# Kernel tuning notes

Measured on AMD Instinct MI355X. Metric: run time of the kernel, lower is better.

## Reference

```python
import jax, jax.numpy as jnp
import numpy as np

B, S, P, H, W, TAG, M, K = 4, 2, 17, 128, 128, 1, 8, 10
PHW = P * H * W
SIGMA, SF = 0.2, 3.0
E_INV = float(np.e ** -1)
EPS = 1e-6


def setup_inputs() -> dict:
    key = jax.random.key(0)
    k1, k2, k3, k4, k5, k6, k7 = jax.random.split(key, 7)
    preds = jax.random.normal(k1, (B, S, (1 + TAG) * P, H, W), jnp.float32)
    gt_masks = jax.random.uniform(k2, (B, H, W), jnp.float32)
    gt_heatmaps = jax.random.uniform(k3, (B, P, H, W), jnp.float32)
    pos = jax.random.uniform(k4, (B, M, P, 2), jnp.float32) * H  # pixel coords
    vis = jax.random.randint(k5, (B, M, P, 1), 0, 2).astype(jnp.float32)
    gt_skeletons = jnp.concatenate([pos, vis], axis=-1)  # [B,M,P,3] = (x, y, vis)
    kp_idx = jax.random.randint(k6, (B, M, P, 1), 0, PHW)
    kp_vis = jax.random.randint(k7, (B, M, P, 1), 0, 2)
    gt_keypoints = jnp.concatenate([kp_idx, kp_vis], axis=-1).astype(jnp.int32)  # [B,M,J,2]
    return {"preds": preds, "gt_masks": gt_masks, "gt_heatmaps": gt_heatmaps,
            "gt_skeletons": gt_skeletons, "gt_keypoints": gt_keypoints}


def _clog(x):
    # torch BCE clamps log at -100
    return jnp.clip(jnp.log(x), -100.0, None)


def _tag_single(pt, kp):
    # pt: [TAG, PHW] tag map for one (image, stack); kp: [M, J, 2] int (flat_idx, vis)
    idx = kp[..., 0]
    vis = (kp[..., 1] > 0).astype(pt.dtype)  # [M, J]
    g = jnp.transpose(pt[:, idx], (1, 2, 0))  # [M, J, TAG]
    cnt = vis.sum(1)  # [M]
    valid = (cnt > 0).astype(pt.dtype)
    safe = jnp.maximum(cnt, 1.0)
    mean_tag = (g * vis[..., None]).sum(1) / safe[:, None]  # [M, TAG]
    # pull: per-person mean over (visible joints x tag dims) of squared deviation
    pull_pp = (((g - mean_tag[:, None]) ** 2) * vis[..., None]).sum((1, 2)) / (safe * TAG)
    num = valid.sum()
    pull = (pull_pp * valid).sum() / (num + EPS)
    d = ((mean_tag[:, None] - mean_tag[None]) ** 2).sum(-1)  # [M, M]
    pm = jnp.exp(-d) * valid[:, None] * valid[None]
    push = (pm.sum() - num) / ((num - 1.0) * num + EPS) * 0.5
    return push, pull


def _forward(preds, gt_masks, gt_heatmaps, gt_skeletons, gt_keypoints):
    hm = preds[:, :, :P]  # [B,S,P,H,W] raw heatmap logits
    prob = jax.nn.sigmoid(hm)
    # ---- detection loss (weighted BCE, per stack) ----
    t = (gt_heatmaps > E_INV).astype(jnp.float32)[:, None]  # [B,1,P,H,W]
    wgt = 10.0 * t + 0.5 * (gt_heatmaps < E_INV).astype(jnp.float32)[:, None]
    x = prob * gt_masks[:, None, None]
    bce = -(t * _clog(x) + (1.0 - t) * _clog(1.0 - x))
    det_loss = (wgt * bce).mean(axis=(0, 2, 3, 4))  # [S]
    # ---- associative embedding push/pull ----
    pred_tag_imgs = preds[:, :, P:(1 + TAG) * P].reshape(B, S, TAG, P, H, W)
    pred_tags = pred_tag_imgs.reshape(B, S, TAG, PHW)
    push, pull = jax.vmap(lambda ptb, kpb: jax.vmap(lambda pt: _tag_single(pt, kpb))(ptb))(
        pred_tags, gt_keypoints)  # each [B,S]
    # ---- keypoint sampling: top-K of flattened probability maps ----
    flat = prob.reshape(B, S, PHW)
    _, topi = jax.lax.top_k(flat, K)  # [B,S,K]
    part = topi // (H * W)
    rem = topi % (H * W)
    xi = rem // W
    yi = rem % W
    pos = jnp.stack([xi, yi], -1).astype(jnp.float32)  # [B,S,K,2]
    # ---- nearest-person matching (faithful to source, incl. vis==1 penalty) ----
    max_dist = float(H + W)
    sk_t = jnp.transpose(gt_skeletons, (0, 2, 1, 3))  # [B,P,M,3]
    pidx = jnp.broadcast_to(part.reshape(B, S * K)[:, :, None, None], (B, S * K, M, 3))
    sk_sel = jnp.take_along_axis(sk_t, pidx, axis=1).reshape(B, S, K, M, 3)
    vispen = max_dist * (sk_sel[..., 2] == 1).astype(jnp.float32)  # [B,S,K,M]
    dvec = vispen[..., None] + sk_sel[..., 1:] - pos[..., None, :]
    dist = jnp.sqrt((dvec ** 2).sum(-1) + 1e-12)
    person_ids = jnp.argmin(dist, axis=-1)  # [B,S,K]
    # ---- gather tag values at sampled locations ----
    pti = jnp.transpose(pred_tag_imgs, (0, 1, 3, 4, 5, 2))  # [B,S,P,H,W,TAG]
    bb = jnp.arange(B)[:, None, None]
    ss = jnp.arange(S)[None, :, None]
    tv = pti[bb, ss, part, xi, yi]  # [B,S,K,TAG]
    # ---- SkeletonGenerator: tag-conditioned soft-argmax ----
    aff = ((pti[:, :, None] - tv[:, :, :, None, None, None, :]) ** 2).sum(-1)  # [B,S,K,P,H,W]
    logits = SF * hm[:, :, None] - aff / (2.0 * SIGMA ** 2)
    wts = jax.nn.softmax(logits.reshape(B, S, K, P, H * W), -1).reshape(B, S, K, P, H, W)
    px = (wts * jnp.arange(H, dtype=jnp.float32)[:, None]).sum((-1, -2))  # [B,S,K,P]
    py = (wts * jnp.arange(W, dtype=jnp.float32)).sum((-1, -2))
    skel = jnp.stack([px, py], -1)  # [B,S,K,P,2]
    gts = gt_skeletons[bb, person_ids]  # [B,S,K,P,3]
    err = jnp.sqrt(((gts[..., :2] - skel) ** 2).sum(-1) + 1e-12) * (gts[..., 2] > 0)
    delta = 0.1
    a = jnp.abs(err)
    small = (a < delta).astype(jnp.float32)
    hub = small * err ** 2 + (1.0 - small) * delta * (a - delta / 2.0)
    skel_loss = hub.mean(-1).mean(-1)  # [B,S]
    # ---- weighted sum (loss_weights = (1,1,1,10)) ----
    return (1.0 * push.mean() + 1.0 * pull.mean() + 1.0 * det_loss.mean()
            + 10.0 * skel_loss.mean())


def reference(preds, gt_masks, gt_heatmaps, gt_skeletons, gt_keypoints):
    return _forward(preds, gt_masks, gt_heatmaps, gt_skeletons, gt_keypoints)
```

## Files before the change

### kernel.cpp

```cpp
#include <hip/hip_runtime.h>
#include <math.h>

#define B_ 4
#define S_ 2
#define P_ 17
#define H_ 128
#define W_ 128
#define M_ 8
#define K_ 10
#define HW_ (H_*W_)
#define PHW_ (P_*HW_)
#define CH_ 34
#define G_ 34
#define C_ (PHW_/G_)
#define E_INV_F 0.36787944117144233f
#define LOG2E 1.4426950408889634f
#define SF_ 3.0f
#define INV2SIG 12.5f
#define MAXDIST 256.0f

#define TOP1_BLOCKS (B_*S_*G_)
#define DET_BLOCKS  544
#define TAG_BLOCKS  (B_*S_)
#define MAIN_BLOCKS (TOP1_BLOCKS + DET_BLOCKS + TAG_BLOCKS)

#define SKEL_CHUNKS 4
#define NBSP (B_*S_*P_)
#define SKEL_BLOCKS (NBSP*SKEL_CHUNKS)

__device__ __forceinline__ unsigned int map32(float f) {
    unsigned int u = __float_as_uint(f);
    unsigned int flip = (unsigned int)((int)u >> 31) | 0x80000000u;
    return u ^ flip;
}

__device__ __forceinline__ void insert10(unsigned long long* a, unsigned long long key) {
    #pragma unroll
    for (int j = 9; j >= 1; --j) {
        unsigned long long am1 = a[j-1];
        a[j] = (key > am1) ? am1 : ((key > a[j]) ? key : a[j]);
    }
    a[0] = (key > a[0]) ? key : a[0];
}

__device__ __forceinline__ void merge10(unsigned long long* a, const unsigned long long* b) {
    #pragma unroll
    for (int t = 0; t < 10; ++t) {
        unsigned long long key = b[t];
        if (key > a[9]) insert10(a, key);
    }
}

__global__ __launch_bounds__(256, 4) void k_main(const float* __restrict__ preds,
                                                 const float* __restrict__ gmask,
                                                 const float* __restrict__ gh,
                                                 const int* __restrict__ kp,
                                                 unsigned long long* __restrict__ cand,
                                                 float* __restrict__ ws_det,
                                                 float* __restrict__ ws_tag) {
    int tid = threadIdx.x;
    if (blockIdx.x < TOP1_BLOCKS) {
        int bs = blockIdx.x / G_;
        int c  = blockIdx.x % G_;
        int wave = tid >> 6, lane = tid & 63;
        const float4* base = (const float4*)(preds + (size_t)bs*CH_*HW_ + (size_t)c*C_);
        unsigned long long a[10];
        #pragma unroll
        for (int j = 0; j < 10; ++j) a[j] = 0ull;
        for (int j = 0; j < 8; ++j) {
            int idx4 = wave*512 + j*64 + lane;
            float4 v = base[idx4];
            unsigned int i0 = (unsigned int)(c*C_ + idx4*4);
            const float* vv = &v.x;
            #pragma unroll
            for (int cc = 0; cc < 4; ++cc) {
                unsigned int key32 = map32(vv[cc]);
                unsigned int thr = (unsigned int)(a[9] >> 32);
                unsigned long long mask = __ballot(key32 >= thr);
                if (mask) {
                    unsigned long long kk =
                        ((unsigned long long)key32 << 32) | (unsigned int)(~(i0 + cc));
                    do {
                        int l = (int)__ffsll(mask) - 1;
                        unsigned long long cnd = __shfl(kk, l);
                        if (cnd > a[9]) insert10(a, cnd);
                        mask &= mask - 1;
                    } while (mask);
                }
            }
        }
        __shared__ unsigned long long smw[4][10];
        if (lane == 0) {
            #pragma unroll
            for (int j = 0; j < 10; ++j) smw[wave][j] = a[j];
        }
        __syncthreads();
        if (tid < 2) {
            unsigned long long x[10], y[10];
            #pragma unroll
            for (int j = 0; j < 10; ++j) { x[j] = smw[tid][j]; y[j] = smw[tid+2][j]; }
            merge10(x, y);
            #pragma unroll
            for (int j = 0; j < 10; ++j) smw[tid][j] = x[j];
        }
        __syncthreads();
        if (tid == 0) {
            unsigned long long x[10], y[10];
            #pragma unroll
            for (int j = 0; j < 10; ++j) { x[j] = smw[0][j]; y[j] = smw[1][j]; }
            merge10(x, y);
            #pragma unroll
            for (int j = 0; j < 10; ++j) cand[(size_t)blockIdx.x*10 + j] = x[j];
        }
    } else if (blockIdx.x < TOP1_BLOCKS + DET_BLOCKS) {
        int dblk = blockIdx.x - TOP1_BLOCKS;
        int t = dblk*256 + tid;
        float acc = 0.0f;
        #pragma unroll
        for (int j = 0; j < 4; ++j) {
            int q = t + j*(DET_BLOCKS*256);
            int hw4 = q & 4095;
            int t1  = q >> 12;
            int p   = t1 % P_;
            int t2  = t1 / P_;
            float4 hm4 = ((const float4*)preds)[(t2*CH_ + p)*4096 + hw4];
            float4 gm4 = ((const float4*)gmask)[(t2>>1)*4096 + hw4];
            float4 gh4 = ((const float4*)gh)[((t2>>1)*P_ + p)*4096 + hw4];
            const float* hmv = &hm4.x; const float* gmv = &gm4.x; const float* ghv4 = &gh4.x;
            #pragma unroll
            for (int cc = 0; cc < 4; ++cc) {
                float hm = hmv[cc];
                float e = exp2f(-fabsf(hm)*LOG2E);
                float r = __builtin_amdgcn_rcpf(1.0f + e);
                float prob = (hm >= 0.0f) ? r : e*r;
                float x = prob * gmv[cc];
                float ghv = ghv4[cc];
                float tt  = (ghv > E_INV_F) ? 1.0f : 0.0f;
                float wgt = 10.0f*tt + ((ghv < E_INV_F) ? 0.5f : 0.0f);
                float lx  = fmaxf(__logf(x),        -100.0f);
                float l1x = fmaxf(__logf(1.0f - x), -100.0f);
                acc += wgt * (-(tt*lx + (1.0f - tt)*l1x));
            }
        }
        #pragma unroll
        for (int off = 32; off > 0; off >>= 1) acc += __shfl_down(acc, off);
        __shared__ float sred[4];
        int wave = tid >> 6, lane = tid & 63;
        if (lane == 0) sred[wave] = acc;
        __syncthreads();
        if (tid == 0) ws_det[dblk] = sred[0] + sred[1] + sred[2] + sred[3];
    } else {
        int bs = blockIdx.x - (TOP1_BLOCKS + DET_BLOCKS);
        int b = bs / S_;
        __shared__ float g[M_*P_];
        __shared__ float vis[M_*P_];
        __shared__ float mean_tag[M_];
        __shared__ float validm[M_];
        __shared__ float pull_pp[M_];
        const float* tagbase = preds + ((size_t)bs*CH_ + P_)*HW_;
        if (tid < M_*P_) {
            int m = tid / P_; int p = tid % P_;
            int off = ((b*M_ + m)*P_ + p)*2;
            int idx = kp[off];
            int v   = kp[off+1];
            g[tid]   = tagbase[idx];
            vis[tid] = (v > 0) ? 1.0f : 0.0f;
        }
        __syncthreads();
        if (tid < M_) {
            float cnt = 0.0f, sum = 0.0f;
            for (int p = 0; p < P_; p++) { cnt += vis[tid*P_+p]; sum += g[tid*P_+p]*vis[tid*P_+p]; }
            float safe = fmaxf(cnt, 1.0f);
            float mt = sum / safe;
            mean_tag[tid] = mt;
            validm[tid] = (cnt > 0.0f) ? 1.0f : 0.0f;
            float pp = 0.0f;
            for (int p = 0; p < P_; p++) { float d = g[tid*P_+p] - mt; pp += d*d*vis[tid*P_+p]; }
            pull_pp[tid] = pp / safe;
        }
        __syncthreads();
        if (tid == 0) {
            float num = 0.0f;
            for (int m = 0; m < M_; m++) num += validm[m];
            float pull = 0.0f;
            for (int m = 0; m < M_; m++) pull += pull_pp[m]*validm[m];
            pull = pull / (num + 1e-6f);
            float pmsum = 0.0f;
            for (int i = 0; i < M_; i++)
                for (int j = 0; j < M_; j++) {
                    float d = mean_tag[i] - mean_tag[j]; d = d*d;
                    pmsum += expf(-d)*validm[i]*validm[j];
                }
            float push = (pmsum - num) / ((num - 1.0f)*num + 1e-6f) * 0.5f;
            ws_tag[bs] = push + pull;
        }
    }
}

__global__ __launch_bounds__(64) void k_top2(const float* __restrict__ preds,
                                             const float* __restrict__ gsk,
                                             const unsigned long long* __restrict__ cand,
                                             float* __restrict__ ws_tv,
                                             int* __restrict__ ws_pid) {
    int bs = blockIdx.x; int b = bs / S_;
    int tid = threadIdx.x;
    __shared__ unsigned long long sm[64*10];
    if (tid < G_) {
        #pragma unroll
        for (int j = 0; j < 10; ++j) sm[tid*10+j] = cand[((size_t)bs*G_ + tid)*10 + j];
    } else {
        #pragma unroll
        for (int j = 0; j < 10; ++j) sm[tid*10+j] = 0ull;
    }
    __syncthreads();
    for (int st = 32; st >= 1; st >>= 1) {
        if (tid < st) {
            unsigned long long x[10], y[10];
            #pragma unroll
            for (int j = 0; j < 10; ++j) { x[j] = sm[tid*10+j]; y[j] = sm[(tid+st)*10+j]; }
            merge10(x, y);
            #pragma unroll
            for (int j = 0; j < 10; ++j) sm[tid*10+j] = x[j];
        }
        __syncthreads();
    }
    if (tid < K_) {
        unsigned long long key = sm[tid];
        unsigned int topi = (unsigned int)(~key);
        int part = topi >> 14;
        int rem  = topi & (HW_-1);
        int xi   = rem >> 7;
        int yi   = rem & (W_-1);
        const float* tagbase = preds + ((size_t)bs*CH_ + P_)*HW_;
        float tv = tagbase[topi];
        float best = INFINITY; int pid = 0;
        for (int m = 0; m < M_; m++) {
            const float* sk = gsk + ((size_t)(b*M_ + m)*P_ + part)*3;
            float sk1 = sk[1], sk2 = sk[2];
            float vp = (sk2 == 1.0f) ? MAXDIST : 0.0f;
            float d0 = vp + sk1 - (float)xi;
            float d1 = vp + sk2 - (float)yi;
            float dist = sqrtf(d0*d0 + d1*d1 + 1e-12f);
            if (dist < best) { best = dist; pid = m; }
        }
        int o = bs*K_ + tid;
        ws_tv[o]  = tv;
        ws_pid[o] = pid;
    }
}

__global__ __launch_bounds__(256, 4) void k_skel(const float* __restrict__ preds,
                                                 const float* __restrict__ ws_tv,
                                                 float* __restrict__ ws_skl,
                                                 float* __restrict__ ws_ssx,
                                                 float* __restrict__ ws_ssy) {
    int bid   = blockIdx.x / SKEL_CHUNKS;
    int chunk = blockIdx.x % SKEL_CHUNKS;
    int p  = bid % P_;
    int bs = bid / P_;
    const float4* hm4 = (const float4*)(preds + ((size_t)bs*CH_ + p)*HW_);
    const float4* tg4 = (const float4*)(preds + ((size_t)bs*CH_ + P_ + p)*HW_);
    float tv[K_];
    #pragma unroll
    for (int k = 0; k < K_; k++) tv[k] = ws_tv[bs*K_ + k];
    float l[K_], sx[K_], sy[K_];
    #pragma unroll
    for (int k = 0; k < K_; k++) { l[k] = 0.0f; sx[k] = 0.0f; sy[k] = 0.0f; }
    int tid = threadIdx.x;
    const float C2 = INV2SIG * LOG2E;
    #pragma unroll
    for (int j = 0; j < 4; ++j) {
        int q = chunk*1024 + j*256 + tid;
        float4 hv = hm4[q];
        float4 tg = tg4[q];
        float h  = (float)(q >> 5);
        float w0 = (float)((q*4) & (W_-1));
        const float* hvv = &hv.x; const float* tgv = &tg.x;
        #pragma unroll
        for (int cc = 0; cc < 4; ++cc) {
            float a2 = (SF_*LOG2E) * hvv[cc];
            float tgc = tgv[cc];
            float w = w0 + (float)cc;
            #pragma unroll
            for (int k = 0; k < K_; k++) {
                float d = tgc - tv[k];
                float e = exp2f(fmaf(-C2, d*d, a2));
                l[k] += e;
                sx[k] = fmaf(e, h, sx[k]);
                sy[k] = fmaf(e, w, sy[k]);
            }
        }
    }
    #pragma unroll
    for (int k = 0; k < K_; k++) {
        for (int off = 32; off > 0; off >>= 1) {
            l[k]  += __shfl_down(l[k],  off);
            sx[k] += __shfl_down(sx[k], off);
            sy[k] += __shfl_down(sy[k], off);
        }
    }
    __shared__ float red[4][K_][3];
    int wave = tid >> 6, lane = tid & 63;
    if (lane == 0) {
        #pragma unroll
        for (int k = 0; k < K_; k++) {
            red[wave][k][0] = l[k]; red[wave][k][1] = sx[k]; red[wave][k][2] = sy[k];
        }
    }
    __syncthreads();
    if (tid < K_) {
        int k = tid;
        float L  = red[0][k][0] + red[1][k][0] + red[2][k][0] + red[3][k][0];
        float SX = red[0][k][1] + red[1][k][1] + red[2][k][1] + red[3][k][1];
        float SY = red[0][k][2] + red[1][k][2] + red[2][k][2] + red[3][k][2];
        int o = blockIdx.x*K_ + k;
        ws_skl[o] = L; ws_ssx[o] = SX; ws_ssy[o] = SY;
    }
}

__global__ __launch_bounds__(256) void k_fin(const float* __restrict__ gsk,
                                             const int* __restrict__ ws_pid,
                                             const float* __restrict__ ws_skl,
                                             const float* __restrict__ ws_ssx,
                                             const float* __restrict__ ws_ssy,
                                             const float* __restrict__ ws_det,
                                             const float* __restrict__ ws_tag,
                                             float* __restrict__ out) {
    int tid = threadIdx.x;
    float acc = 0.0f;
    for (int i = tid; i < DET_BLOCKS; i += 256) acc += ws_det[i];
    acc *= (1.0f/(float)(B_*S_*P_*HW_));
    if (tid < B_*S_) acc += ws_tag[tid] * (1.0f/(float)(B_*S_));
    for (int idx = tid; idx < NBSP*K_; idx += 256) {
        int bid = idx / K_;
        int k   = idx % K_;
        int p  = bid % P_;
        int bs = bid / P_;
        int b  = bs / S_;
        float L = 0.0f, SX = 0.0f, SY = 0.0f;
        #pragma unroll
        for (int c = 0; c < SKEL_CHUNKS; ++c) {
            int o = (bid*SKEL_CHUNKS + c)*K_ + k;
            L += ws_skl[o]; SX += ws_ssx[o]; SY += ws_ssy[o];
        }
        float px = SX / L, py = SY / L;
        int pid = ws_pid[bs*K_ + k];
        const float* g = gsk + ((size_t)(b*M_ + pid)*P_ + p)*3;
        float d0 = g[0] - px, d1 = g[1] - py;
        float gate = (g[2] > 0.0f) ? 1.0f : 0.0f;
        float err = sqrtf(d0*d0 + d1*d1 + 1e-12f) * gate;
        float hub = (err < 0.1f) ? err*err : 0.1f*(err - 0.05f);
        acc += hub * (10.0f/(float)(B_*S_*K_*P_));
    }
    #pragma unroll
    for (int off = 32; off > 0; off >>= 1) acc += __shfl_down(acc, off);
    __shared__ float sred[4];
    int wave = tid >> 6, lane = tid & 63;
    if (lane == 0) sred[wave] = acc;
    __syncthreads();
    if (tid == 0) out[0] = sred[0] + sred[1] + sred[2] + sred[3];
}

extern "C" void kernel_launch(void* const* d_in, const int* in_sizes, int n_in,
                              void* d_out, int out_size, void* d_ws, size_t ws_size,
                              hipStream_t stream) {
    (void)in_sizes; (void)n_in; (void)out_size; (void)ws_size;
    const float* preds = (const float*)d_in[0];
    const float* gmask = (const float*)d_in[1];
    const float* gh    = (const float*)d_in[2];
    const float* gsk   = (const float*)d_in[3];
    const int*   gkp   = (const int*)d_in[4];
    float* out = (float*)d_out;
    unsigned long long* cand = (unsigned long long*)d_ws;
    float* ws_tv  = (float*)(cand + (size_t)B_*S_*G_*10);
    int*   ws_pid = (int*)(ws_tv + (size_t)B_*S_*K_);
    float* ws_skl = (float*)(ws_pid + (size_t)B_*S_*K_);
    float* ws_ssx = ws_skl + (size_t)SKEL_BLOCKS*K_;
    float* ws_ssy = ws_ssx + (size_t)SKEL_BLOCKS*K_;
    float* ws_det = ws_ssy + (size_t)SKEL_BLOCKS*K_;
    float* ws_tag = ws_det + DET_BLOCKS;

    hipLaunchKernelGGL(k_main, dim3(MAIN_BLOCKS), dim3(256), 0, stream,
                       preds, gmask, gh, gkp, cand, ws_det, ws_tag);
    hipLaunchKernelGGL(k_top2, dim3(B_*S_),       dim3(64),  0, stream,
                       preds, gsk, cand, ws_tv, ws_pid);
    hipLaunchKernelGGL(k_skel, dim3(SKEL_BLOCKS), dim3(256), 0, stream,
                       preds, ws_tv, ws_skl, ws_ssx, ws_ssy);
    hipLaunchKernelGGL(k_fin,  dim3(1),           dim3(256), 0, stream,
                       gsk, ws_pid, ws_skl, ws_ssx, ws_ssy, ws_det, ws_tag, out);
}
```

Measured before the change: 130.2 us.

## Fuse top-k candidate scan with detection BCE in one pass over heatmaps

Merges the top-10 candidate search and the weighted BCE detection loss into the same blocks, so each heatmap element is loaded once and used for both. Each thread now keeps its own top-10 list, updated for every element, and the lists are combined by a shared-memory tree merge. This replaces the wave-level ballot/shuffle filter, which only inserted values above the current threshold. The tag push/pull work moves from k_main into the second kernel next to the top-k finalisation. The intent is to remove a duplicate read of preds and the idle imbalance of the tag blocks. The cost is more per-element insert work, heavier register use, 20 KB of shared memory per block, and an 8-level merge with barriers.

```diff
diff --git a/kernel.cpp b/kernel.cpp
--- a/kernel.cpp
+++ b/kernel.cpp
@@ -12,18 +12,14 @@
 #define PHW_ (P_*HW_)
 #define CH_ 34
 #define G_ 34
-#define C_ (PHW_/G_)
+#define C_ 8192
 #define E_INV_F 0.36787944117144233f
 #define LOG2E 1.4426950408889634f
 #define SF_ 3.0f
 #define INV2SIG 12.5f
 #define MAXDIST 256.0f
 
-#define TOP1_BLOCKS (B_*S_*G_)
-#define DET_BLOCKS  544
-#define TAG_BLOCKS  (B_*S_)
-#define MAIN_BLOCKS (TOP1_BLOCKS + DET_BLOCKS + TAG_BLOCKS)
-
+#define MAIN_BLOCKS (B_*S_*G_)
 #define SKEL_CHUNKS 4
 #define NBSP (B_*S_*P_)
 #define SKEL_BLOCKS (NBSP*SKEL_CHUNKS)
@@ -54,163 +50,133 @@
 __global__ __launch_bounds__(256, 4) void k_main(const float* __restrict__ preds,
                                                  const float* __restrict__ gmask,
                                                  const float* __restrict__ gh,
-                                                 const int* __restrict__ kp,
                                                  unsigned long long* __restrict__ cand,
-                                                 float* __restrict__ ws_det,
-                                                 float* __restrict__ ws_tag) {
-    int tid = threadIdx.x;
-    if (blockIdx.x < TOP1_BLOCKS) {
-        int bs = blockIdx.x / G_;
-        int c  = blockIdx.x % G_;
-        int wave = tid >> 6, lane = tid & 63;
-        const float4* base = (const float4*)(preds + (size_t)bs*CH_*HW_ + (size_t)c*C_);
-        unsigned long long a[10];
+                                                 float* __restrict__ ws_det) {
+    int bs = blockIdx.x / G_;
+    int c  = blockIdx.x % G_;
+    int p    = c >> 1;
+    int half = c & 1;
+    int b    = bs / S_;
+    int tid  = threadIdx.x;
+    const float4* base = (const float4*)(preds + (size_t)bs*CH_*HW_ + (size_t)c*C_);
+    const float4* gm4p = (const float4*)(gmask) + (size_t)b*4096 + half*2048;
+    const float4* gh4p = (const float4*)(gh) + ((size_t)b*P_ + p)*4096 + half*2048;
+
+    unsigned long long a[10];
+    #pragma unroll
+    for (int j = 0; j < 10; ++j) a[j] = 0ull;
+    float det_acc = 0.0f;
+
+    #pragma unroll
+    for (int j = 0; j < 8; ++j) {
+        int q = j*256 + tid;
+        float4 hv = base[q];
+        float4 gm = gm4p[q];
+        float4 gv = gh4p[q];
+        unsigned int i0 = (unsigned int)(c*C_ + q*4);
+        const float* hvv = &hv.x; const float* gmv = &gm.x; const float* ghv4 = &gv.x;
         #pragma unroll
-        for (int j = 0; j < 10; ++j) a[j] = 0ull;
-        for (int j = 0; j < 8; ++j) {
-            int idx4 = wave*512 + j*64 + lane;
-            float4 v = base[idx4];
-            unsigned int i0 = (unsigned int)(c*C_ + idx4*4);
-            const float* vv = &v.x;
-            #pragma unroll
-            for (int cc = 0; cc < 4; ++cc) {
-                unsigned int key32 = map32(vv[cc]);
-                unsigned int thr = (unsigned int)(a[9] >> 32);
-                unsigned long long mask = __ballot(key32 >= thr);
-                if (mask) {
-                    unsigned long long kk =
-                        ((unsigned long long)key32 << 32) | (unsigned int)(~(i0 + cc));
-                    do {
-                        int l = (int)__ffsll(mask) - 1;
-                        unsigned long long cnd = __shfl(kk, l);
-                        if (cnd > a[9]) insert10(a, cnd);
-                        mask &= mask - 1;
-                    } while (mask);
-                }
-            }
-        }
-        __shared__ unsigned long long smw[4][10];
-        if (lane == 0) {
-            #pragma unroll
-            for (int j = 0; j < 10; ++j) smw[wave][j] = a[j];
+        for (int cc = 0; cc < 4; ++cc) {
+            float hm = hvv[cc];
+            unsigned long long key =
+                ((unsigned long long)map32(hm) << 32) | (unsigned int)(~(i0 + cc));
+            insert10(a, key);
+            float e = exp2f(-fabsf(hm)*LOG2E);
+            float r = __builtin_amdgcn_rcpf(1.0f + e);
+            float prob = (hm >= 0.0f) ? r : e*r;
+            float x = prob * gmv[cc];
+            float ghv = ghv4[cc];
+            float tt  = (ghv > E_INV_F) ? 1.0f : 0.0f;
+            float wgt = 10.0f*tt + ((ghv < E_INV_F) ? 0.5f : 0.0f);
+            float lx  = fmaxf(__logf(x),        -100.0f);
+            float l1x = fmaxf(__logf(1.0f - x), -100.0f);
+            det_acc += wgt * (-(tt*lx + (1.0f - tt)*l1x));
+        }
+    }
+    #pragma unroll
+    for (int off = 32; off > 0; off >>= 1) det_acc += __shfl_down(det_acc, off);
+    __shared__ float sred[4];
+    int wave = tid >> 6, lane = tid & 63;
+    if (lane == 0) sred[wave] = det_acc;
+    __shared__ unsigned long long sm[256*10];
+    #pragma unroll
+    for (int j = 0; j < 10; ++j) sm[tid*10+j] = a[j];
+    __syncthreads();
+    if (tid == 0) ws_det[blockIdx.x] = sred[0] + sred[1] + sred[2] + sred[3];
+    for (int st = 128; st >= 1; st >>= 1) {
+        if (tid < st) {
+            unsigned long long x[10], y[10];
+            #pragma unroll
+            for (int j = 0; j < 10; ++j) { x[j] = sm[tid*10+j]; y[j] = sm[(tid+st)*10+j]; }
+            merge10(x, y);
+            #pragma unroll
+            for (int j = 0; j < 10; ++j) sm[tid*10+j] = x[j];
         }
         __syncthreads();
-        if (tid < 2) {
-            unsigned long long x[10], y[10];
-            #pragma unroll
-            for (int j = 0; j < 10; ++j) { x[j] = smw[tid][j]; y[j] = smw[tid+2][j]; }
-            merge10(x, y);
-            #pragma unroll
-            for (int j = 0; j < 10; ++j) smw[tid][j] = x[j];
-        }
-        __syncthreads();
-        if (tid == 0) {
-            unsigned long long x[10], y[10];
-            #pragma unroll
-            for (int j = 0; j < 10; ++j) { x[j] = smw[0][j]; y[j] = smw[1][j]; }
-            merge10(x, y);
-            #pragma unroll
-            for (int j = 0; j < 10; ++j) cand[(size_t)blockIdx.x*10 + j] = x[j];
-        }
-    } else if (blockIdx.x < TOP1_BLOCKS + DET_BLOCKS) {
-        int dblk = blockIdx.x - TOP1_BLOCKS;
-        int t = dblk*256 + tid;
-        float acc = 0.0f;
-        #pragma unroll
-        for (int j = 0; j < 4; ++j) {
-            int q = t + j*(DET_BLOCKS*256);
-            int hw4 = q & 4095;
-            int t1  = q >> 12;
-            int p   = t1 % P_;
-            int t2  = t1 / P_;
-            float4 hm4 = ((const float4*)preds)[(t2*CH_ + p)*4096 + hw4];
-            float4 gm4 = ((const float4*)gmask)[(t2>>1)*4096 + hw4];
-            float4 gh4 = ((const float4*)gh)[((t2>>1)*P_ + p)*4096 + hw4];
-            const float* hmv = &hm4.x; const float* gmv = &gm4.x; const float* ghv4 = &gh4.x;
-            #pragma unroll
-            for (int cc = 0; cc < 4; ++cc) {
-                float hm = hmv[cc];
-                float e = exp2f(-fabsf(hm)*LOG2E);
-                float r = __builtin_amdgcn_rcpf(1.0f + e);
-                float prob = (hm >= 0.0f) ? r : e*r;
-                float x = prob * gmv[cc];
-                float ghv = ghv4[cc];
-                float tt  = (ghv > E_INV_F) ? 1.0f : 0.0f;
-                float wgt = 10.0f*tt + ((ghv < E_INV_F) ? 0.5f : 0.0f);
-                float lx  = fmaxf(__logf(x),        -100.0f);
-                float l1x = fmaxf(__logf(1.0f - x), -100.0f);
-                acc += wgt * (-(tt*lx + (1.0f - tt)*l1x));
-            }
-        }
-        #pragma unroll
-        for (int off = 32; off > 0; off >>= 1) acc += __shfl_down(acc, off);
-        __shared__ float sred[4];
-        int wave = tid >> 6, lane = tid & 63;
-        if (lane == 0) sred[wave] = acc;
-        __syncthreads();
-        if (tid == 0) ws_det[dblk] = sred[0] + sred[1] + sred[2] + sred[3];
-    } else {
-        int bs = blockIdx.x - (TOP1_BLOCKS + DET_BLOCKS);
-        int b = bs / S_;
-        __shared__ float g[M_*P_];
-        __shared__ float vis[M_*P_];
-        __shared__ float mean_tag[M_];
-        __shared__ float validm[M_];
-        __shared__ float pull_pp[M_];
-        const float* tagbase = preds + ((size_t)bs*CH_ + P_)*HW_;
-        if (tid < M_*P_) {
-            int m = tid / P_; int p = tid % P_;
-            int off = ((b*M_ + m)*P_ + p)*2;
-            int idx = kp[off];
-            int v   = kp[off+1];
-            g[tid]   = tagbase[idx];
-            vis[tid] = (v > 0) ? 1.0f : 0.0f;
-        }
-        __syncthreads();
-        if (tid < M_) {
-            float cnt = 0.0f, sum = 0.0f;
-            for (int p = 0; p < P_; p++) { cnt += vis[tid*P_+p]; sum += g[tid*P_+p]*vis[tid*P_+p]; }
-            float safe = fmaxf(cnt, 1.0f);
-            float mt = sum / safe;
-            mean_tag[tid] = mt;
-            validm[tid] = (cnt > 0.0f) ? 1.0f : 0.0f;
-            float pp = 0.0f;
-            for (int p = 0; p < P_; p++) { float d = g[tid*P_+p] - mt; pp += d*d*vis[tid*P_+p]; }
-            pull_pp[tid] = pp / safe;
-        }
-        __syncthreads();
-        if (tid == 0) {
-            float num = 0.0f;
-            for (int m = 0; m < M_; m++) num += validm[m];
-            float pull = 0.0f;
-            for (int m = 0; m < M_; m++) pull += pull_pp[m]*validm[m];
-            pull = pull / (num + 1e-6f);
-            float pmsum = 0.0f;
-            for (int i = 0; i < M_; i++)
-                for (int j = 0; j < M_; j++) {
-                    float d = mean_tag[i] - mean_tag[j]; d = d*d;
-                    pmsum += expf(-d)*validm[i]*validm[j];
-                }
-            float push = (pmsum - num) / ((num - 1.0f)*num + 1e-6f) * 0.5f;
-            ws_tag[bs] = push + pull;
-        }
-    }
-}
-
-__global__ __launch_bounds__(64) void k_top2(const float* __restrict__ preds,
-                                             const float* __restrict__ gsk,
-                                             const unsigned long long* __restrict__ cand,
-                                             float* __restrict__ ws_tv,
-                                             int* __restrict__ ws_pid) {
+    }
+    if (tid < 10) cand[(size_t)blockIdx.x*10 + tid] = sm[tid];
+}
+
+__global__ __launch_bounds__(256) void k_tt(const float* __restrict__ preds,
+                                            const float* __restrict__ gsk,
+                                            const int* __restrict__ kp,
+                                            const unsigned long long* __restrict__ cand,
+                                            float* __restrict__ ws_tag,
+                                            float* __restrict__ ws_tv,
+                                            int* __restrict__ ws_pid) {
     int bs = blockIdx.x; int b = bs / S_;
     int tid = threadIdx.x;
+    const float* tagbase = preds + ((size_t)bs*CH_ + P_)*HW_;
+    __shared__ float g[M_*P_];
+    __shared__ float vis[M_*P_];
+    __shared__ float mean_tag[M_];
+    __shared__ float validm[M_];
+    __shared__ float pull_pp[M_];
+    if (tid < M_*P_) {
+        int m = tid / P_; int pp = tid % P_;
+        int off = ((b*M_ + m)*P_ + pp)*2;
+        int idx = kp[off];
+        int v   = kp[off+1];
+        g[tid]   = tagbase[idx];
+        vis[tid] = (v > 0) ? 1.0f : 0.0f;
+    }
+    __syncthreads();
+    if (tid < M_) {
+        float cnt = 0.0f, sum = 0.0f;
+        for (int pp = 0; pp < P_; pp++) { cnt += vis[tid*P_+pp]; sum += g[tid*P_+pp]*vis[tid*P_+pp]; }
+        float safe = fmaxf(cnt, 1.0f);
+        float mt = sum / safe;
+        mean_tag[tid] = mt;
+        validm[tid] = (cnt > 0.0f) ? 1.0f : 0.0f;
+        float pl = 0.0f;
+        for (int pp = 0; pp < P_; pp++) { float d = g[tid*P_+pp] - mt; pl += d*d*vis[tid*P_+pp]; }
+        pull_pp[tid] = pl / safe;
+    }
+    __syncthreads();
+    if (tid == 0) {
+        float num = 0.0f;
+        for (int m = 0; m < M_; m++) num += validm[m];
+        float pull = 0.0f;
+        for (int m = 0; m < M_; m++) pull += pull_pp[m]*validm[m];
+        pull = pull / (num + 1e-6f);
+        float pmsum = 0.0f;
+        for (int i = 0; i < M_; i++)
+            for (int j = 0; j < M_; j++) {
+                float d = mean_tag[i] - mean_tag[j]; d = d*d;
+                pmsum += expf(-d)*validm[i]*validm[j];
+            }
+        float push = (pmsum - num) / ((num - 1.0f)*num + 1e-6f) * 0.5f;
+        ws_tag[bs] = push + pull;
+    }
     __shared__ unsigned long long sm[64*10];
-    if (tid < G_) {
-        #pragma unroll
-        for (int j = 0; j < 10; ++j) sm[tid*10+j] = cand[((size_t)bs*G_ + tid)*10 + j];
-    } else {
-        #pragma unroll
-        for (int j = 0; j < 10; ++j) sm[tid*10+j] = 0ull;
+    if (tid < 64) {
+        if (tid < G_) {
+            #pragma unroll
+            for (int j = 0; j < 10; ++j) sm[tid*10+j] = cand[((size_t)bs*G_ + tid)*10 + j];
+        } else {
+            #pragma unroll
+            for (int j = 0; j < 10; ++j) sm[tid*10+j] = 0ull;
+        }
     }
     __syncthreads();
     for (int st = 32; st >= 1; st >>= 1) {
@@ -231,7 +197,6 @@
         int rem  = topi & (HW_-1);
         int xi   = rem >> 7;
         int yi   = rem & (W_-1);
-        const float* tagbase = preds + ((size_t)bs*CH_ + P_)*HW_;
         float tv = tagbase[topi];
         float best = INFINITY; int pid = 0;
         for (int m = 0; m < M_; m++) {
@@ -328,7 +293,7 @@
                                              float* __restrict__ out) {
     int tid = threadIdx.x;
     float acc = 0.0f;
-    for (int i = tid; i < DET_BLOCKS; i += 256) acc += ws_det[i];
+    for (int i = tid; i < MAIN_BLOCKS; i += 256) acc += ws_det[i];
     acc *= (1.0f/(float)(B_*S_*P_*HW_));
     if (tid < B_*S_) acc += ws_tag[tid] * (1.0f/(float)(B_*S_));
     for (int idx = tid; idx < NBSP*K_; idx += 256) {
@@ -378,12 +343,12 @@
     float* ws_ssx = ws_skl + (size_t)SKEL_BLOCKS*K_;
     float* ws_ssy = ws_ssx + (size_t)SKEL_BLOCKS*K_;
     float* ws_det = ws_ssy + (size_t)SKEL_BLOCKS*K_;
-    float* ws_tag = ws_det + DET_BLOCKS;
+    float* ws_tag = ws_det + MAIN_BLOCKS;
 
     hipLaunchKernelGGL(k_main, dim3(MAIN_BLOCKS), dim3(256), 0, stream,
-                       preds, gmask, gh, gkp, cand, ws_det, ws_tag);
-    hipLaunchKernelGGL(k_top2, dim3(B_*S_),       dim3(64),  0, stream,
-                       preds, gsk, cand, ws_tv, ws_pid);
+                       preds, gmask, gh, cand, ws_det);
+    hipLaunchKernelGGL(k_tt,   dim3(B_*S_),       dim3(256), 0, stream,
+                       preds, gsk, gkp, cand, ws_tag, ws_tv, ws_pid);
     hipLaunchKernelGGL(k_skel, dim3(SKEL_BLOCKS), dim3(256), 0, stream,
                        preds, ws_tv, ws_skl, ws_ssx, ws_ssy);
     hipLaunchKernelGGL(k_fin,  dim3(1),           dim3(256), 0, stream,
```

New measurement: 140.6 us. 8.0% more time.
